# Performance work log

Measured on AMD Instinct MI355X. Metric: run time of the kernel, lower is better.

Reference implementation:

```python
import jax, jax.numpy as jnp
import numpy as np

SN, H, W, BN = 4, 128, 128, 65536


def _perspective(fov_deg=60.0, near=0.1, far=100.0):
    f = 1.0 / np.tan(np.deg2rad(fov_deg) / 2.0)
    p = np.zeros((4, 4), np.float32)
    p[0, 0] = f
    p[1, 1] = f
    p[2, 2] = (far + near) / (near - far)
    p[2, 3] = 2.0 * far * near / (near - far)
    p[3, 2] = -1.0
    return p


def setup_inputs() -> dict:
    key = jax.random.key(0)
    ks = jax.random.split(key, 7)
    depth = jax.random.uniform(ks[0], (1, SN, 1, H, W), jnp.float32)
    normal = jax.random.normal(ks[1], (1, SN, 3, H, W), jnp.float32)
    indices = jax.random.randint(ks[2], (BN,), 0, SN, jnp.int32)
    proj = jnp.asarray(_perspective()[None])  # (1,4,4)
    x = jax.random.randint(ks[3], (BN,), 0, W, jnp.int32)
    y = jax.random.randint(ks[4], (BN,), 0, H, jnp.int32)
    d = jax.random.normal(ks[5], (BN, 3), jnp.float32)
    depth_start = jax.random.uniform(ks[6], (BN,), jnp.float32, minval=0.2, maxval=0.8)
    return dict(depth=depth, normal=normal, indices=indices, proj=proj,
                x=x, y=y, d=d, depth_start=depth_start)


def _transform(pos, mat):
    # pos: (bn,3), mat: (4,4) -> homogeneous transform + perspective divide
    pos4 = jnp.concatenate([pos, jnp.ones((pos.shape[0], 1), pos.dtype)], axis=1)
    out = pos4 @ mat.T
    return out[:, :3] / out[:, 3:4]


def _march_next(cur_pos, ray_dir, cur_x, cur_y, h, w, step_x, step_y):
    next_bx = (cur_x + step_x).astype(cur_pos.dtype) / w
    next_by = (cur_y + step_y).astype(cur_pos.dtype) / h
    ncb = jnp.stack([next_bx, 1.0 - next_by], axis=1)          # (bn,2)
    step_ratio = (ncb - cur_pos[:, :2]) / ray_dir[:, :2]       # (bn,2)
    take_y = step_ratio[:, 0] > step_ratio[:, 1]
    dx = jnp.where(take_y, 0, step_x)
    dy = jnp.where(take_y, step_y, 0)
    new_pos = cur_pos + ray_dir * jnp.min(step_ratio, axis=1, keepdims=True)
    return new_pos, dx, dy


def _ssrt(depth, normal, indices, proj, x, y, d, depth_start):
    h, w = depth.shape[2], depth.shape[3]
    bn = x.shape[0]
    unproj = jnp.linalg.inv(proj)
    uv = jnp.stack([(x.astype(jnp.float32) + 0.5) / w,
                    1.0 - (y.astype(jnp.float32) + 0.5) / h], axis=1) * 2.0 - 1.0
    ds = depth_start * 2.0 - 1.0
    proj_pos = jnp.stack([uv[:, 0], uv[:, 1], ds], axis=1)     # (bn,3) NDC
    view_pos = _transform(proj_pos, unproj)
    d_proj = _transform(view_pos + d * 0.001, proj) - proj_pos # projected ray dir
    cur_pos = (proj_pos + 1.0) * 0.5                           # [0,1]^3 screen space
    step_x = jnp.where(d_proj[:, 0] >= 0, 1, -1).astype(x.dtype)
    step_y = jnp.where(d_proj[:, 1] >= 0, -1, 1).astype(y.dtype)
    cur_pos, dx, dy = _march_next(cur_pos, d_proj, x, y, h, w, step_x, step_y)
    cur_x = x + dx
    cur_y = y + dy
    mask = jnp.zeros((bn,), bool)
    results = jnp.zeros((bn, 2), x.dtype)
    dz = jnp.zeros((bn, 1), jnp.float32)

    def cond(state):
        p, _, _, m, _, _ = state
        within = (p[:, 0] >= 0) & (p[:, 0] <= 1) & (p[:, 1] >= 0) & (p[:, 1] <= 1) & (p[:, 2] > 0) & (p[:, 2] < 1)
        return jnp.any(within) & (~jnp.all(m))

    def body(state):
        pos, cx, cy, m, res, dzv = state
        within = (cx >= 0) & (cx < w) & (cy >= 0) & (cy < h)
        xs = jnp.clip(cx, 0, w - 1)
        ys = jnp.clip(cy, 0, h - 1)
        z = depth[indices, 0, ys, xs]                  # (bn,) depth-buffer gather
        nrm = normal[indices, :, ys, xs]               # (bn,3) normal gather
        pz = pos[:, 2]
        hit = within & (pz >= z) & (jnp.sum(d * nrm, axis=1) <= 0) & (~m)
        m = m | hit
        res = jnp.where(hit[:, None], jnp.stack([cx, cy], axis=-1), res)
        dzv = jnp.where(hit[:, None], (pz - z)[:, None], dzv)
        pos, ddx, ddy = _march_next(pos, d_proj, cx, cy, h, w, step_x, step_y)
        return (pos, cx + ddx, cy + ddy, m, res, dzv)

    state = jax.lax.while_loop(cond, body, (cur_pos, cur_x, cur_y, mask, results, dz))
    return state[4], state[3], state[5]


def reference(depth, normal, indices, proj, x, y, d, depth_start):
    return _ssrt(depth[0], normal[0], indices, proj[0], x, y, d, depth_start)
```

## Files before the change

kernel.cpp:

```cpp
#include <hip/hip_runtime.h>
#include <math.h>

#pragma clang fp contract(off)

#define BN 65536
#define SN 4
#define HH 128
#define WW 128

typedef float v4f __attribute__((ext_vector_type(4)));
typedef int v4i __attribute__((ext_vector_type(4)));
__device__ v4f __llvm_buffer_load_v4f32(v4i rsrc, int voffset, int soffset,
                                        int aux) __asm("llvm.amdgcn.raw.buffer.load.v4f32");

__device__ __forceinline__ void inv4(const float* P, float U[4][4]) {
#pragma clang fp contract(off)
    float a = P[10];
    float b = P[11];
    float ra = 1.0f / a;
    float l32 = P[14] * ra;
    float t = l32 * b;
    float u33 = 0.0f - t;
    float rf0 = 1.0f / P[0];
    float rf1 = 1.0f / P[5];
    float ru  = 1.0f / u33;
#pragma unroll
    for (int i = 0; i < 4; i++)
#pragma unroll
        for (int j = 0; j < 4; j++) U[i][j] = 0.0f;
    U[0][0] = rf0;
    U[1][1] = rf1;
    float x3c2 = (0.0f - l32) * ru;
    float y2c2 = fmaf(0.0f - b, x3c2, 1.0f);
    U[2][2] = y2c2 * ra;
    U[3][2] = x3c2;
    float x3c3 = ru;
    float y2c3 = 0.0f - (b * x3c3);
    U[2][3] = y2c3 * ra;
    U[3][3] = x3c3;
}

__device__ __forceinline__ void xform(const float M[4][4], float x, float y, float z,
                                      float& ox, float& oy, float& oz) {
#pragma clang fp contract(off)
    float o[4];
#pragma unroll
    for (int i = 0; i < 4; i++) {
        float acc = x * M[i][0];
        acc = acc + y * M[i][1];
        acc = acc + z * M[i][2];
        acc = acc + M[i][3];
        o[i] = acc;
    }
    ox = o[0] / o[3];
    oy = o[1] / o[3];
    oz = o[2] / o[3];
}

struct RS {
    float p0, p1, p2, d0, d1, d2;
    float y0, y1;
    float fx, cy1;
    float sxf, syf;
    float da, db, dc, hdz;
    int cx, cy, sx, sy, base, B, hoff, hk;
    bool still, testing, hit;
};

__device__ __forceinline__ void make_ray(RS& S, int r, const float* proj,
                                         const int* idxA, const int* xA, const int* yA,
                                         const float* dA, const float* dsA) {
#pragma clang fp contract(off)
    float P[4][4];
#pragma unroll
    for (int i = 0; i < 16; i++) ((float*)P)[i] = proj[i];
    float U[4][4];
    inv4(proj, U);
    int xi = xA[r], yi = yA[r];
    float t0 = ((float)xi + 0.5f) / 128.0f;
    float t1 = 1.0f - ((float)yi + 0.5f) / 128.0f;
    float ux = t0 * 2.0f - 1.0f;
    float uy = t1 * 2.0f - 1.0f;
    float ds = dsA[r] * 2.0f - 1.0f;
    float vx, vy, vz;
    xform(U, ux, uy, ds, vx, vy, vz);
    float ex = vx + dA[3 * r + 0] * 0.001f;
    float ey = vy + dA[3 * r + 1] * 0.001f;
    float ez = vz + dA[3 * r + 2] * 0.001f;
    float qx, qy, qz;
    xform(P, ex, ey, ez, qx, qy, qz);
    S.d0 = qx - ux;
    S.d1 = qy - uy;
    S.d2 = qz - ds;
    S.p0 = (ux + 1.0f) * 0.5f;
    S.p1 = (uy + 1.0f) * 0.5f;
    S.p2 = (ds + 1.0f) * 0.5f;
    S.sx = (S.d0 >= 0.0f) ? 1 : -1;
    S.sy = (S.d1 >= 0.0f) ? -1 : 1;
    S.cx = xi;
    S.cy = yi;
    {
        float nbx = (float)(S.cx + S.sx) / 128.0f;
        float nby = (float)(S.cy + S.sy) / 128.0f;
        float c1 = 1.0f - nby;
        float s0 = (nbx - S.p0) / S.d0;
        float s1 = (c1 - S.p1) / S.d1;
        bool ty = s0 > s1;
        float t = ty ? s1 : s0;
        if (s1 != s1) t = s1;
        S.p0 = S.p0 + S.d0 * t;
        S.p1 = S.p1 + S.d1 * t;
        S.p2 = S.p2 + S.d2 * t;
        if (ty) S.cy += S.sy; else S.cx += S.sx;
    }
    S.y0 = 1.0f / S.d0;
    S.y1 = 1.0f / S.d1;
    S.fx  = (float)(S.cx + S.sx) / 128.0f;
    S.cy1 = 1.0f - (float)(S.cy + S.sy) / 128.0f;
    S.sxf = (float)S.sx * 0.0078125f;
    S.syf = (float)S.sy * 0.0078125f;
    S.da = dA[3 * r + 0]; S.db = dA[3 * r + 1]; S.dc = dA[3 * r + 2];
    S.base = idxA[r] * (HH * WW);
    S.B = 0; S.hoff = 0; S.hk = 0; S.hdz = 0.0f;
    S.still = true; S.testing = true; S.hit = false;
}

__global__ __launch_bounds__(256) void k_pack(const float* __restrict__ depth,
                                              const float* __restrict__ normal,
                                              float4* __restrict__ tab, int* ws) {
    int t = blockIdx.x * 256 + threadIdx.x;
    if (t == 0) ws[0] = 0;
    int s = t >> 14;
    int c = t & 16383;
    float4 v;
    v.x = depth[t];
    v.y = normal[s * 3 * HH * WW + c];
    v.z = normal[s * 3 * HH * WW + HH * WW + c];
    v.w = normal[s * 3 * HH * WW + 2 * HH * WW + c];
    tab[t] = v;
}

__global__ void k_zero(int* ws) { ws[0] = 0; }

template <bool PACKED>
__global__ __launch_bounds__(256, 1) void k_march8(const float* __restrict__ depth,
                                                   const float* __restrict__ normal,
                                                   const float4* __restrict__ tab,
                                                   const int* idxA, const float* proj,
                                                   const int* xA, const int* yA,
                                                   const float* dA, const float* dsA,
                                                   float* out, int* ws) {
#pragma clang fp contract(off)
    int r = blockIdx.x * 256 + threadIdx.x;
    RS S;
    make_ray(S, r, proj, idxA, xA, yA, dA, dsA);
    const float* dep = depth + S.base;
    const float* nrm = normal + 3 * S.base;

    v4i rsrc;
    {
        unsigned long long p = (unsigned long long)(const void*)tab;
        rsrc.x = (int)(p & 0xFFFFFFFFull);
        rsrc.y = (int)(p >> 32);
        rsrc.z = SN * HH * WW * 16;
        rsrc.w = 0x00020000;
    }

#define DECL_SLOT(u) \
    float z##u = 0.0f, a##u = 0.0f, b##u = 0.0f, c##u = 0.0f, q##u = 0.0f; \
    int o##u = 0; bool v##u = false;
    DECL_SLOT(0) DECL_SLOT(1) DECL_SLOT(2) DECL_SLOT(3)
    DECL_SLOT(4) DECL_SLOT(5) DECL_SLOT(6) DECL_SLOT(7)
#undef DECL_SLOT

#define CONSUME(u, kcons) { \
        float t0 = S.da * a##u; \
        float t1 = S.db * b##u; \
        float t2 = S.dc * c##u; \
        float dotv = (t0 + t1) + t2; \
        bool hc = v##u && (q##u >= z##u) && (dotv <= 0.0f) && !S.hit; \
        S.hit = S.hit || hc; \
        S.hoff = hc ? o##u : S.hoff; \
        S.hk   = hc ? (kcons) : S.hk; \
        float dzn = q##u - z##u; \
        S.hdz  = hc ? dzn : S.hdz; \
        v##u = false; }

#define BOXCHK(inow) { \
        bool ib = (S.p0 >= 0.0f) && (S.p0 <= 1.0f) && \
                  (S.p1 >= 0.0f) && (S.p1 <= 1.0f) && \
                  (S.p2 > 0.0f) && (S.p2 < 1.0f); \
        S.still = S.still && ib; \
        S.B = S.still ? ((inow) + 1) : S.B; }

#define MARCH {  \
        float x0 = S.fx - S.p0; \
        float x1 = S.cy1 - S.p1; \
        float q0a = x0 * S.y0; \
        float rra = fmaf(-S.d0, q0a, x0); \
        float s0v = fmaf(rra, S.y0, q0a); \
        float q0b = x1 * S.y1; \
        float rrb = fmaf(-S.d1, q0b, x1); \
        float s1v = fmaf(rrb, S.y1, q0b); \
        bool ty = s0v > s1v; \
        float t = ty ? s1v : s0v; \
        t = (s1v != s1v) ? s1v : t; \
        float m0 = S.d0 * t; S.p0 = S.p0 + m0; \
        float m1 = S.d1 * t; S.p1 = S.p1 + m1; \
        float m2 = S.d2 * t; S.p2 = S.p2 + m2; \
        S.cx  += ty ? 0 : S.sx; \
        S.cy  += ty ? S.sy : 0; \
        S.fx  += ty ? 0.0f : S.sxf; \
        S.cy1 -= ty ? S.syf : 0.0f; }

#define STEP(u, inow) { \
        CONSUME(u, (inow) - 8) \
        BOXCHK(inow) \
        { bool inpix = ((unsigned)S.cx < (unsigned)WW) && ((unsigned)S.cy < (unsigned)HH); \
          bool dead = (S.d2 <= 0.0f) && (S.p2 < 0.0f);    \
          S.testing = S.testing && inpix && !S.hit && !dead; \
          int off = S.cy * WW + S.cx; \
          v##u = S.testing; o##u = off; q##u = S.p2; \
          if (PACKED) { \
              int voff = S.testing ? ((S.base + off) << 4) : 0x40000000; \
              v4f vv = __llvm_buffer_load_v4f32(rsrc, voff, 0, 0); \
              z##u = vv.x; a##u = vv.y; b##u = vv.z; c##u = vv.w; \
          } else if (S.testing) { \
              z##u = dep[off]; \
              a##u = nrm[off]; \
              b##u = nrm[HH * WW + off]; \
              c##u = nrm[2 * HH * WW + off]; \
          } } \
        MARCH \
        __builtin_amdgcn_sched_barrier(0); }

    int i = 0;
    while (i < 4096) {
        STEP(0, i)     STEP(1, i + 1) STEP(2, i + 2) STEP(3, i + 3)
        STEP(4, i + 4) STEP(5, i + 5) STEP(6, i + 6) STEP(7, i + 7)
        i += 8;
        if (!__any(S.testing)) break;
    }
    CONSUME(0, i - 8) CONSUME(1, i - 7) CONSUME(2, i - 6) CONSUME(3, i - 5)
    CONSUME(4, i - 4) CONSUME(5, i - 3) CONSUME(6, i - 2) CONSUME(7, i - 1)

    while (i < 4096 && __any(S.still)) {
#pragma unroll
        for (int u = 0; u < 8; ++u) {
            BOXCHK(i + u)
            MARCH
        }
        i += 8;
    }
#undef STEP
#undef MARCH
#undef BOXCHK
#undef CONSUME

    int pk = S.hit ? (S.hoff | (1 << 14)) : 0;
    out[2 * r]      = (float)pk;
    out[2 * r + 1]  = (float)S.hk;
    out[3 * BN + r] = S.hdz;

    int Bm = S.B;
    for (int o = 32; o; o >>= 1) {
        int v = __shfl_down(Bm, o, 64);
        Bm = Bm > v ? Bm : v;
    }
    if ((threadIdx.x & 63) == 0) atomicMax(ws, Bm);
}

__global__ __launch_bounds__(256) void k_final(float* out, const int* ws) {
    int r = blockIdx.x * 256 + threadIdx.x;
    int N = ws[0];
    int pk = (int)out[2 * r];
    int k  = (int)out[2 * r + 1];
    float dzv = out[3 * BN + r];
    bool hit = (pk >> 14) & 1;
    bool ok = hit && (k < N);
    int rx = pk & 127, ry = (pk >> 7) & 127;
    out[2 * r]      = ok ? (float)rx : 0.0f;
    out[2 * r + 1]  = ok ? (float)ry : 0.0f;
    out[2 * BN + r] = ok ? 1.0f : 0.0f;
    out[3 * BN + r] = ok ? dzv : 0.0f;
}

extern "C" void kernel_launch(void* const* d_in, const int* in_sizes, int n_in,
                              void* d_out, int out_size, void* d_ws, size_t ws_size,
                              hipStream_t stream) {
    const float* depth = (const float*)d_in[0];
    const float* normal = (const float*)d_in[1];
    const int* indices = (const int*)d_in[2];
    const float* proj = (const float*)d_in[3];
    const int* x = (const int*)d_in[4];
    const int* y = (const int*)d_in[5];
    const float* d = (const float*)d_in[6];
    const float* ds = (const float*)d_in[7];
    float* out = (float*)d_out;
    int* ws = (int*)d_ws;

    const size_t tab_off = 64;
    const size_t need = tab_off + (size_t)SN * HH * WW * 16;
    float4* tab = (float4*)((char*)d_ws + tab_off);

    if (ws_size >= need) {
        k_pack<<<(SN * HH * WW) / 256, 256, 0, stream>>>(depth, normal, tab, ws);
        k_march8<true><<<BN / 256, 256, 0, stream>>>(depth, normal, tab, indices,
                                                     proj, x, y, d, ds, out, ws);
    } else {
        k_zero<<<1, 1, 0, stream>>>(ws);
        k_march8<false><<<BN / 256, 256, 0, stream>>>(depth, normal, tab, indices,
                                                      proj, x, y, d, ds, out, ws);
    }
    k_final<<<BN / 256, 256, 0, stream>>>(out, ws);
}
```

Before: 43.67 us.

## Fuse pack, march and finalize into one cooperative kernel with grid syncs

Replaces the three-kernel sequence (pack table, march rays, finalize) with a single cooperative launch that packs, grid-syncs, marches, reduces the max step count, grid-syncs again and writes final outputs directly. This is meant to remove two kernel launch overheads and the intermediate round-trip of packed results through global memory. It relies on all 256 blocks being co-resident and falls back to the old path if the cooperative launch fails. Grid-wide barriers add their own synchronization cost, and the slowest block now gates the whole grid before the final writes.

```diff
diff --git a/kernel.cpp b/kernel.cpp
--- a/kernel.cpp
+++ b/kernel.cpp
@@ -1,5 +1,8 @@
 #include <hip/hip_runtime.h>
+#include <hip/hip_cooperative_groups.h>
 #include <math.h>
+
+namespace cg = cooperative_groups;
 
 #pragma clang fp contract(off)
 
@@ -125,54 +128,6 @@
     S.still = true; S.testing = true; S.hit = false;
 }
 
-__global__ __launch_bounds__(256) void k_pack(const float* __restrict__ depth,
-                                              const float* __restrict__ normal,
-                                              float4* __restrict__ tab, int* ws) {
-    int t = blockIdx.x * 256 + threadIdx.x;
-    if (t == 0) ws[0] = 0;
-    int s = t >> 14;
-    int c = t & 16383;
-    float4 v;
-    v.x = depth[t];
-    v.y = normal[s * 3 * HH * WW + c];
-    v.z = normal[s * 3 * HH * WW + HH * WW + c];
-    v.w = normal[s * 3 * HH * WW + 2 * HH * WW + c];
-    tab[t] = v;
-}
-
-__global__ void k_zero(int* ws) { ws[0] = 0; }
-
-template <bool PACKED>
-__global__ __launch_bounds__(256, 1) void k_march8(const float* __restrict__ depth,
-                                                   const float* __restrict__ normal,
-                                                   const float4* __restrict__ tab,
-                                                   const int* idxA, const float* proj,
-                                                   const int* xA, const int* yA,
-                                                   const float* dA, const float* dsA,
-                                                   float* out, int* ws) {
-#pragma clang fp contract(off)
-    int r = blockIdx.x * 256 + threadIdx.x;
-    RS S;
-    make_ray(S, r, proj, idxA, xA, yA, dA, dsA);
-    const float* dep = depth + S.base;
-    const float* nrm = normal + 3 * S.base;
-
-    v4i rsrc;
-    {
-        unsigned long long p = (unsigned long long)(const void*)tab;
-        rsrc.x = (int)(p & 0xFFFFFFFFull);
-        rsrc.y = (int)(p >> 32);
-        rsrc.z = SN * HH * WW * 16;
-        rsrc.w = 0x00020000;
-    }
-
-#define DECL_SLOT(u) \
-    float z##u = 0.0f, a##u = 0.0f, b##u = 0.0f, c##u = 0.0f, q##u = 0.0f; \
-    int o##u = 0; bool v##u = false;
-    DECL_SLOT(0) DECL_SLOT(1) DECL_SLOT(2) DECL_SLOT(3)
-    DECL_SLOT(4) DECL_SLOT(5) DECL_SLOT(6) DECL_SLOT(7)
-#undef DECL_SLOT
-
 #define CONSUME(u, kcons) { \
         float t0 = S.da * a##u; \
         float t1 = S.db * b##u; \
@@ -213,11 +168,157 @@
         S.fx  += ty ? 0.0f : S.sxf; \
         S.cy1 -= ty ? S.syf : 0.0f; }
 
+#define DECL_SLOT(u) \
+    float z##u = 0.0f, a##u = 0.0f, b##u = 0.0f, c##u = 0.0f, q##u = 0.0f; \
+    int o##u = 0; bool v##u = false;
+
+__global__ __launch_bounds__(256) void k_pack(const float* __restrict__ depth,
+                                              const float* __restrict__ normal,
+                                              float4* __restrict__ tab, int* ws) {
+    int t = blockIdx.x * 256 + threadIdx.x;
+    if (t == 0) ws[0] = 0;
+    int s = t >> 14;
+    int c = t & 16383;
+    float4 v;
+    v.x = depth[t];
+    v.y = normal[s * 3 * HH * WW + c];
+    v.z = normal[s * 3 * HH * WW + HH * WW + c];
+    v.w = normal[s * 3 * HH * WW + 2 * HH * WW + c];
+    tab[t] = v;
+}
+
+__global__ void k_zero(int* ws) { ws[0] = 0; }
+
+__global__ __launch_bounds__(256, 1) void k_fused(const float* __restrict__ depth,
+                                                  const float* __restrict__ normal,
+                                                  float4* __restrict__ tab,
+                                                  const int* idxA, const float* proj,
+                                                  const int* xA, const int* yA,
+                                                  const float* dA, const float* dsA,
+                                                  float* out, int* ws) {
+#pragma clang fp contract(off)
+    cg::grid_group grid = cg::this_grid();
+    int gtid = blockIdx.x * 256 + threadIdx.x;
+
+    {
+        int t = gtid;
+        if (t == 0) ws[0] = 0;
+        int s = t >> 14;
+        int c = t & 16383;
+        float4 v;
+        v.x = depth[t];
+        v.y = normal[s * 3 * HH * WW + c];
+        v.z = normal[s * 3 * HH * WW + HH * WW + c];
+        v.w = normal[s * 3 * HH * WW + 2 * HH * WW + c];
+        tab[t] = v;
+    }
+    __threadfence();
+    grid.sync();
+
+    int r = gtid;
+    RS S;
+    make_ray(S, r, proj, idxA, xA, yA, dA, dsA);
+
+    v4i rsrc;
+    {
+        unsigned long long p = (unsigned long long)(const void*)tab;
+        rsrc.x = (int)(p & 0xFFFFFFFFull);
+        rsrc.y = (int)(p >> 32);
+        rsrc.z = SN * HH * WW * 16;
+        rsrc.w = 0x00020000;
+    }
+
+    DECL_SLOT(0) DECL_SLOT(1) DECL_SLOT(2) DECL_SLOT(3)
+    DECL_SLOT(4) DECL_SLOT(5) DECL_SLOT(6) DECL_SLOT(7)
+
 #define STEP(u, inow) { \
         CONSUME(u, (inow) - 8) \
         BOXCHK(inow) \
         { bool inpix = ((unsigned)S.cx < (unsigned)WW) && ((unsigned)S.cy < (unsigned)HH); \
           bool dead = (S.d2 <= 0.0f) && (S.p2 < 0.0f);    \
+          S.testing = S.testing && inpix && !S.hit && !dead; \
+          int off = S.cy * WW + S.cx; \
+          v##u = S.testing; o##u = off; q##u = S.p2; \
+          { int voff = S.testing ? ((S.base + off) << 4) : 0x40000000; \
+            v4f vv = __llvm_buffer_load_v4f32(rsrc, voff, 0, 0); \
+            z##u = vv.x; a##u = vv.y; b##u = vv.z; c##u = vv.w; } } \
+        MARCH \
+        __builtin_amdgcn_sched_barrier(0); }
+
+    int i = 0;
+    while (i < 4096) {
+        STEP(0, i)     STEP(1, i + 1) STEP(2, i + 2) STEP(3, i + 3)
+        STEP(4, i + 4) STEP(5, i + 5) STEP(6, i + 6) STEP(7, i + 7)
+        i += 8;
+        if (!__any(S.testing)) break;
+    }
+    CONSUME(0, i - 8) CONSUME(1, i - 7) CONSUME(2, i - 6) CONSUME(3, i - 5)
+    CONSUME(4, i - 4) CONSUME(5, i - 3) CONSUME(6, i - 2) CONSUME(7, i - 1)
+
+    while (i < 4096 && __any(S.still)) {
+#pragma unroll
+        for (int u = 0; u < 8; ++u) {
+            BOXCHK(i + u)
+            MARCH
+        }
+        i += 8;
+    }
+#undef STEP
+
+    int Bm = S.B;
+    for (int o = 32; o; o >>= 1) {
+        int v = __shfl_down(Bm, o, 64);
+        Bm = Bm > v ? Bm : v;
+    }
+    if ((threadIdx.x & 63) == 0) atomicMax(ws, Bm);
+
+    __threadfence();
+    grid.sync();
+
+    __shared__ int smN;
+    if (threadIdx.x == 0) smN = atomicMax(ws, 0);
+    __syncthreads();
+    int N = smN;
+    bool ok = S.hit && (S.hk < N);
+    int rx = S.hoff & 127, ry = (S.hoff >> 7) & 127;
+    out[2 * r]      = ok ? (float)rx : 0.0f;
+    out[2 * r + 1]  = ok ? (float)ry : 0.0f;
+    out[2 * BN + r] = ok ? 1.0f : 0.0f;
+    out[3 * BN + r] = ok ? S.hdz : 0.0f;
+}
+
+template <bool PACKED>
+__global__ __launch_bounds__(256, 1) void k_march8(const float* __restrict__ depth,
+                                                   const float* __restrict__ normal,
+                                                   const float4* __restrict__ tab,
+                                                   const int* idxA, const float* proj,
+                                                   const int* xA, const int* yA,
+                                                   const float* dA, const float* dsA,
+                                                   float* out, int* ws) {
+#pragma clang fp contract(off)
+    int r = blockIdx.x * 256 + threadIdx.x;
+    RS S;
+    make_ray(S, r, proj, idxA, xA, yA, dA, dsA);
+    const float* dep = depth + S.base;
+    const float* nrm = normal + 3 * S.base;
+
+    v4i rsrc;
+    {
+        unsigned long long p = (unsigned long long)(const void*)tab;
+        rsrc.x = (int)(p & 0xFFFFFFFFull);
+        rsrc.y = (int)(p >> 32);
+        rsrc.z = SN * HH * WW * 16;
+        rsrc.w = 0x00020000;
+    }
+
+    DECL_SLOT(0) DECL_SLOT(1) DECL_SLOT(2) DECL_SLOT(3)
+    DECL_SLOT(4) DECL_SLOT(5) DECL_SLOT(6) DECL_SLOT(7)
+
+#define STEP(u, inow) { \
+        CONSUME(u, (inow) - 8) \
+        BOXCHK(inow) \
+        { bool inpix = ((unsigned)S.cx < (unsigned)WW) && ((unsigned)S.cy < (unsigned)HH); \
+          bool dead = (S.d2 <= 0.0f) && (S.p2 < 0.0f); \
           S.testing = S.testing && inpix && !S.hit && !dead; \
           int off = S.cy * WW + S.cx; \
           v##u = S.testing; o##u = off; q##u = S.p2; \
@@ -253,9 +354,6 @@
         i += 8;
     }
 #undef STEP
-#undef MARCH
-#undef BOXCHK
-#undef CONSUME
 
     int pk = S.hit ? (S.hoff | (1 << 14)) : 0;
     out[2 * r]      = (float)pk;
@@ -304,13 +402,22 @@
     float4* tab = (float4*)((char*)d_ws + tab_off);
 
     if (ws_size >= need) {
-        k_pack<<<(SN * HH * WW) / 256, 256, 0, stream>>>(depth, normal, tab, ws);
-        k_march8<true><<<BN / 256, 256, 0, stream>>>(depth, normal, tab, indices,
-                                                     proj, x, y, d, ds, out, ws);
+        void* args[] = {(void*)&depth, (void*)&normal, (void*)&tab, (void*)&indices,
+                        (void*)&proj, (void*)&x, (void*)&y, (void*)&d, (void*)&ds,
+                        (void*)&out, (void*)&ws};
+        hipError_t err = hipLaunchCooperativeKernel((const void*)k_fused,
+                                                    dim3(BN / 256), dim3(256),
+                                                    args, 0, stream);
+        if (err != hipSuccess) {
+            k_pack<<<(SN * HH * WW) / 256, 256, 0, stream>>>(depth, normal, tab, ws);
+            k_march8<true><<<BN / 256, 256, 0, stream>>>(depth, normal, tab, indices,
+                                                         proj, x, y, d, ds, out, ws);
+            k_final<<<BN / 256, 256, 0, stream>>>(out, ws);
+        }
     } else {
         k_zero<<<1, 1, 0, stream>>>(ws);
         k_march8<false><<<BN / 256, 256, 0, stream>>>(depth, normal, tab, indices,
                                                       proj, x, y, d, ds, out, ws);
-    }
-    k_final<<<BN / 256, 256, 0, stream>>>(out, ws);
-}
+        k_final<<<BN / 256, 256, 0, stream>>>(out, ws);
+    }
+}
```

After: 158.3 us. 262% more time.
